# Kernel optimization log

Hardware: AMD Instinct MI355X
Metric: run time of the kernel (lower is better)

Reference implementation:

```python
import jax, jax.numpy as jnp
import numpy as np
from jax import lax

T, D = 8192, 128          # sequence length, feature dim
N_INIT = 100              # burn-in length
RENORM = 0.1
A, B, C = 0.5, 0.9, 0.1   # weighted_dot scaling args: uv = A*gram + B*k_prev + C
EPS = 1e-6                # keep arcsin arg strictly inside (-1, 1)


def kernel_fn(uv, uu, vv):
    # erf-network arcsin kernel
    denom = jnp.sqrt((1.0 + 2.0 * uu) * (1.0 + 2.0 * vv))
    arg = jnp.clip(2.0 * uv / denom, -1.0 + EPS, 1.0 - EPS)
    return (2.0 / jnp.pi) * jnp.arcsin(arg)


def dot_fn(g, k):
    return A * g + B * k + C


def setup_inputs() -> dict:
    key = jax.random.key(0)
    data = jax.random.normal(key, (T, D), dtype=jnp.float32) / np.float32(np.sqrt(D))
    return {"data": data}


def reference(data):
    X = data[:-1]                      # [N, D], N = T - 1
    N = X.shape[0]
    gram = jnp.dot(X, X.T)             # [N, N]
    diag = jnp.diag(gram)              # [N]

    # --- diagonal recursion: scalar carry over time ---
    def diag_step(k_prev, g):
        uv = dot_fn(g, k_prev)
        k = kernel_fn(uv, uv, uv)
        return k, k

    k_diag_final, k_diag = lax.scan(diag_step, jnp.float32(0.0), diag)
    k_diag_shift = jnp.pad(k_diag[:-1], (1, 0))   # shift by one step
    uu = dot_fn(diag, k_diag_shift)               # [N]

    # --- full kernel recursion: carry is a length-N row, shifted each step ---
    def row_step(k_prev, inputs):
        g_row, vv = inputs
        k_prev = jnp.pad(k_prev[:-1], (1, 0))
        uv = dot_fn(g_row, k_prev)
        k = kernel_fn(uv, uu, vv)
        return k, k

    k_final, k_train = lax.scan(row_step, jnp.zeros((N,), jnp.float32), (gram, uu))

    k_train = k_train[N_INIT - 1:, N_INIT - 1:] + RENORM * gram[N_INIT - 1:, N_INIT - 1:]
    return (k_train, uu, k_final, k_diag_final)
```

## Files before the change

kernel.cpp:

```cpp
#include <hip/hip_runtime.h>
#include <hip/hip_fp16.h>

#define N_ROWS 8191
#define NO 8092
#define GSTRIDE 8192
#define SEG 512
#define WARM 96

#define OUT_UU  65480464ul
#define OUT_KF  65488655ul
#define OUT_KDF 65496846ul

#define WS_XB   134217728ul
#define WS_DIAG 136314880ul
#define WS_Q    136347648ul

typedef short bf16x8 __attribute__((ext_vector_type(8)));
typedef float f32x4  __attribute__((ext_vector_type(4)));

__device__ __forceinline__ float asin_core(float a) {
    float ax  = fabsf(a);
    bool  big = ax > 0.5f;
    float z   = big ? 0.5f * (1.0f - ax) : ax * ax;
    float x   = big ? sqrtf(z) : ax;
    float p = fmaf(z, 4.2163199048e-2f, 2.4181311049e-2f);
    p = fmaf(p, z, 4.5470025998e-2f);
    p = fmaf(p, z, 7.4953002686e-2f);
    p = fmaf(p, z, 1.6666752422e-1f);
    p = fmaf(p * z, x, x);
    float r = big ? fmaf(-2.0f, p, 1.57079632679489662f) : p;
    return copysignf(r, a);
}

__device__ __forceinline__ float kstep(float g, float kp, float m) {
    float uv  = fmaf(0.5f, g, fmaf(0.9f, kp, 0.1f));
    float arg = uv * m;
    arg = fminf(fmaxf(arg, -0.999999f), 0.999999f);
    return 0.63661977236758134f * asin_core(arg);
}

__device__ __forceinline__ unsigned short f2bf(float f) {
    unsigned int u = __float_as_uint(f);
    u = (u + 0x7FFFu + ((u >> 16) & 1u)) >> 16;
    return (unsigned short)u;
}

__global__ void k_convert(const float* __restrict__ X, unsigned short* __restrict__ Xb) {
    int idx = blockIdx.x * 256 + threadIdx.x;
    float v = (idx < N_ROWS * 128) ? X[idx] : 0.0f;
    Xb[idx] = f2bf(v);
}

__global__ void k_diag(const float* __restrict__ X, float* __restrict__ diag) {
    int gwave = (blockIdx.x * 256 + threadIdx.x) >> 6;
    int lane  = threadIdx.x & 63;
    if (gwave >= N_ROWS) return;
    const float2* row = (const float2*)(X + (size_t)gwave * 128);
    float2 v = row[lane];
    float s = v.x * v.x + v.y * v.y;
    #pragma unroll
    for (int off = 32; off > 0; off >>= 1) s += __shfl_xor(s, off, 64);
    if (lane == 0) diag[gwave] = s;
}

__global__ void k_scan_diag(const float* __restrict__ diag, float* __restrict__ q,
                            float* __restrict__ d_out) {
    int tid = threadIdx.x;
    int t0  = tid * 32;
    int tw  = max(0, t0 - 32);
    int te  = min(t0 + 32, N_ROWS);
    float kp = 0.0f;
    for (int t = tw; t < te; ++t) {
        float dg = diag[t];
        float uv = fmaf(0.5f, dg, fmaf(0.9f, kp, 0.1f));
        float s  = fabsf(fmaf(2.0f, uv, 1.0f));
        float arg = (uv + uv) / s;
        arg = fminf(fmaxf(arg, -0.999999f), 0.999999f);
        float k = 0.63661977236758134f * asin_core(arg);
        if (t >= t0) {
            d_out[OUT_UU + t] = uv;
            q[t] = 1.0f / sqrtf(s);
            if (t == N_ROWS - 1) d_out[OUT_KDF] = k;
        }
        kp = k;
    }
}

#define GP 136
__global__ __launch_bounds__(256) void k_gemm(const unsigned short* __restrict__ Xb,
                                              __half* __restrict__ gram) {
    int bi = blockIdx.y, bj = blockIdx.x;
    if (bj < bi) return;
    __shared__ short As[128 * GP];
    __shared__ short Bs[128 * GP];
    int tid = threadIdx.x;
    const uint4* ga = (const uint4*)(Xb + (size_t)bi * 128 * 128);
    const uint4* gb = (const uint4*)(Xb + (size_t)bj * 128 * 128);
    #pragma unroll
    for (int p = 0; p < 8; ++p) {
        int chunk = tid + p * 256;
        int row = chunk >> 4, c8 = chunk & 15;
        uint4 va = ga[row * 16 + c8];
        *(uint4*)&As[row * GP + c8 * 8] = va;
        uint4 vb = gb[row * 16 + c8];
        *(uint4*)&Bs[row * GP + c8 * 8] = vb;
    }
    __syncthreads();

    int lane = tid & 63, wave = tid >> 6;
    int wm = wave & 1, wn = wave >> 1;
    int lr = lane & 15, lk = lane >> 4;
    f32x4 acc[4][4];
    #pragma unroll
    for (int mi = 0; mi < 4; ++mi)
        #pragma unroll
        for (int ni = 0; ni < 4; ++ni) acc[mi][ni] = (f32x4){0.f, 0.f, 0.f, 0.f};

    #pragma unroll
    for (int kc = 0; kc < 4; ++kc) {
        bf16x8 a[4], b[4];
        #pragma unroll
        for (int mi = 0; mi < 4; ++mi)
            a[mi] = *(bf16x8*)&As[(wm * 64 + mi * 16 + lr) * GP + kc * 32 + lk * 8];
        #pragma unroll
        for (int ni = 0; ni < 4; ++ni)
            b[ni] = *(bf16x8*)&Bs[(wn * 64 + ni * 16 + lr) * GP + kc * 32 + lk * 8];
        #pragma unroll
        for (int mi = 0; mi < 4; ++mi)
            #pragma unroll
            for (int ni = 0; ni < 4; ++ni)
                acc[mi][ni] = __builtin_amdgcn_mfma_f32_16x16x32_bf16(a[mi], b[ni], acc[mi][ni], 0, 0, 0);
    }

    int row0 = (lane >> 4) * 4, col = lane & 15;
    #pragma unroll
    for (int mi = 0; mi < 4; ++mi) {
        #pragma unroll
        for (int ni = 0; ni < 4; ++ni) {
            size_t gi = (size_t)bi * 128 + wm * 64 + mi * 16 + row0;
            size_t gj = (size_t)bj * 128 + wn * 64 + ni * 16 + col;
            f32x4 v = acc[mi][ni];
            #pragma unroll
            for (int r = 0; r < 4; ++r)
                gram[(gi + r) * GSTRIDE + gj] = __float2half(v[r]);
        }
    }
}

__global__ __launch_bounds__(256) void k_scan_main(const __half* __restrict__ gram,
                                                   const float* __restrict__ q,
                                                   float* __restrict__ d_out) {
    int c = blockIdx.x * 256 + threadIdx.x;
    if (c > NO - 1) return;
    int tlim = N_ROWS - c;
    int t0 = 99 + blockIdx.y * SEG;
    if (t0 >= tlim) return;
    int tend = min(t0 + SEG, tlim);
    int tw = t0 - WARM;

    float kp = 0.0f;
    size_t gidx = (size_t)tw * GSTRIDE + tw + c;
    #pragma unroll 4
    for (int t = tw; t < t0; ++t, gidx += (GSTRIDE + 1)) {
        float g = __half2float(gram[gidx]);
        float m = 2.0f * q[t] * q[t + c];
        kp = kstep(g, kp, m);
    }
    size_t oidx = (size_t)(t0 - 99) * NO + (t0 + c - 99);
    #pragma unroll 4
    for (int t = t0; t < tend; ++t, gidx += (GSTRIDE + 1), oidx += (NO + 1)) {
        float g = __half2float(gram[gidx]);
        float m = 2.0f * q[t] * q[t + c];
        kp = kstep(g, kp, m);
        d_out[oidx] = fmaf(0.1f, g, kp);
    }
    if (tend == tlim) d_out[OUT_KF + (tlim - 1)] = kp;
}

__global__ void k_short_diag(const __half* __restrict__ gram, const float* __restrict__ q,
                             float* __restrict__ d_out) {
    int l = threadIdx.x;
    if (l > 98) return;
    int c = NO + l;
    int tl = N_ROWS - c;
    float kp = 0.0f;
    size_t gidx = (size_t)c;
    for (int t = 0; t < tl; ++t, gidx += (GSTRIDE + 1)) {
        float g = __half2float(gram[gidx]);
        float m = 2.0f * q[t] * q[t + c];
        kp = kstep(g, kp, m);
    }
    d_out[OUT_KF + (tl - 1)] = kp;
}

__global__ __launch_bounds__(256) void k_mirror(float* __restrict__ out) {
    int tc = blockIdx.x, tr = blockIdx.y;
    if (tr < tc) return;
    __shared__ float tile[32][33];
    int tx = threadIdx.x, ty = threadIdx.y;
    int sr0 = tc * 32, sc0 = tr * 32;
    #pragma unroll
    for (int k2 = 0; k2 < 32; k2 += 8) {
        int r = sr0 + ty + k2, cc = sc0 + tx;
        if (r < NO && cc < NO)
            tile[ty + k2][tx] = out[(size_t)r * NO + cc];
    }
    __syncthreads();
    int dr0 = tr * 32, dc0 = tc * 32;
    #pragma unroll
    for (int k2 = 0; k2 < 32; k2 += 8) {
        int r = dr0 + ty + k2, cc = dc0 + tx;
        if (r < NO && cc < NO && r > cc)
            out[(size_t)r * NO + cc] = tile[tx][ty + k2];
    }
}

extern "C" void kernel_launch(void* const* d_in, const int* in_sizes, int n_in,
                              void* d_out, int out_size, void* d_ws, size_t ws_size,
                              hipStream_t stream) {
    const float* X = (const float*)d_in[0];
    float* out = (float*)d_out;
    char* ws = (char*)d_ws;
    __half* gram = (__half*)ws;
    unsigned short* Xb = (unsigned short*)(ws + WS_XB);
    float* diag = (float*)(ws + WS_DIAG);
    float* q = (float*)(ws + WS_Q);

    k_convert<<<dim3(4096), dim3(256), 0, stream>>>(X, Xb);
    k_diag<<<dim3(2048), dim3(256), 0, stream>>>(X, diag);
    k_scan_diag<<<dim3(1), dim3(256), 0, stream>>>(diag, q, out);
    k_gemm<<<dim3(64, 64), dim3(256), 0, stream>>>(Xb, gram);
    k_scan_main<<<dim3(32, 16), dim3(256), 0, stream>>>(gram, q, out);
    k_short_diag<<<dim3(1), dim3(128), 0, stream>>>(gram, q, out);
    k_mirror<<<dim3(253, 253), dim3(32, 8), 0, stream>>>(out);
}
```

Measured before the change: 521.9 us.

## Store gram diagonally skewed, vectorize scan per lane, fuse prep, widen mirror tiles

The GEMM now writes the gram matrix in a skewed layout (row t, offset c = j - i), so the main scan reads contiguous ushort4 vectors per row instead of strided diagonal elements. Each lane now handles four columns, and q values are carried in registers. Segment and warmup lengths shrink to give more parallel blocks. The convert and diag kernels are fused into one, and the mirror transpose uses 64x64 tiles with float4 accesses. Shorter warmup may lose accuracy, and the skewed writes from the GEMM are scattered and less coalesced.

```diff
diff --git a/kernel.cpp b/kernel.cpp
--- a/kernel.cpp
+++ b/kernel.cpp
@@ -4,8 +4,8 @@
 #define N_ROWS 8191
 #define NO 8092
 #define GSTRIDE 8192
-#define SEG 512
-#define WARM 96
+#define SEG 128
+#define WARM 24
 
 #define OUT_UU  65480464ul
 #define OUT_KF  65488655ul
@@ -17,12 +17,16 @@
 
 typedef short bf16x8 __attribute__((ext_vector_type(8)));
 typedef float f32x4  __attribute__((ext_vector_type(4)));
+
+__device__ __forceinline__ float h2f(unsigned short u) {
+    __half_raw r; r.x = u; return __half2float(__half(r));
+}
 
 __device__ __forceinline__ float asin_core(float a) {
     float ax  = fabsf(a);
     bool  big = ax > 0.5f;
     float z   = big ? 0.5f * (1.0f - ax) : ax * ax;
-    float x   = big ? sqrtf(z) : ax;
+    float x   = big ? __builtin_amdgcn_sqrtf(z) : ax;
     float p = fmaf(z, 4.2163199048e-2f, 2.4181311049e-2f);
     p = fmaf(p, z, 4.5470025998e-2f);
     p = fmaf(p, z, 7.4953002686e-2f);
@@ -45,22 +49,20 @@
     return (unsigned short)u;
 }
 
-__global__ void k_convert(const float* __restrict__ X, unsigned short* __restrict__ Xb) {
-    int idx = blockIdx.x * 256 + threadIdx.x;
-    float v = (idx < N_ROWS * 128) ? X[idx] : 0.0f;
-    Xb[idx] = f2bf(v);
-}
-
-__global__ void k_diag(const float* __restrict__ X, float* __restrict__ diag) {
-    int gwave = (blockIdx.x * 256 + threadIdx.x) >> 6;
-    int lane  = threadIdx.x & 63;
-    if (gwave >= N_ROWS) return;
-    const float2* row = (const float2*)(X + (size_t)gwave * 128);
-    float2 v = row[lane];
-    float s = v.x * v.x + v.y * v.y;
-    #pragma unroll
-    for (int off = 32; off > 0; off >>= 1) s += __shfl_xor(s, off, 64);
-    if (lane == 0) diag[gwave] = s;
+__global__ void k_prep(const float* __restrict__ X, unsigned short* __restrict__ Xb,
+                       float* __restrict__ diag) {
+    int gw = (blockIdx.x * 256 + threadIdx.x) >> 6;
+    int lane = threadIdx.x & 63;
+    float2 v = make_float2(0.0f, 0.0f);
+    if (gw < N_ROWS) v = ((const float2*)(X + (size_t)gw * 128))[lane];
+    ushort2 b; b.x = f2bf(v.x); b.y = f2bf(v.y);
+    ((ushort2*)(Xb + (size_t)gw * 128))[lane] = b;
+    if (gw < N_ROWS) {
+        float s = v.x * v.x + v.y * v.y;
+        #pragma unroll
+        for (int off = 32; off > 0; off >>= 1) s += __shfl_xor(s, off, 64);
+        if (lane == 0) diag[gw] = s;
+    }
 }
 
 __global__ void k_scan_diag(const float* __restrict__ diag, float* __restrict__ q,
@@ -84,6 +86,7 @@
         }
         kp = k;
     }
+    for (int j = tid; j < 1024; j += 256) q[N_ROWS + j] = 1.0f;
 }
 
 #define GP 136
@@ -137,81 +140,147 @@
     for (int mi = 0; mi < 4; ++mi) {
         #pragma unroll
         for (int ni = 0; ni < 4; ++ni) {
-            size_t gi = (size_t)bi * 128 + wm * 64 + mi * 16 + row0;
-            size_t gj = (size_t)bj * 128 + wn * 64 + ni * 16 + col;
+            int gi0 = bi * 128 + wm * 64 + mi * 16 + row0;
+            int gj  = bj * 128 + wn * 64 + ni * 16 + col;
             f32x4 v = acc[mi][ni];
             #pragma unroll
-            for (int r = 0; r < 4; ++r)
-                gram[(gi + r) * GSTRIDE + gj] = __float2half(v[r]);
-        }
-    }
-}
-
-__global__ __launch_bounds__(256) void k_scan_main(const __half* __restrict__ gram,
-                                                   const float* __restrict__ q,
-                                                   float* __restrict__ d_out) {
-    int c = blockIdx.x * 256 + threadIdx.x;
-    if (c > NO - 1) return;
-    int tlim = N_ROWS - c;
+            for (int r = 0; r < 4; ++r) {
+                int gi = gi0 + r, c = gj - gi;
+                if (c >= 0)
+                    gram[(size_t)gi * GSTRIDE + c] = __float2half(v[r]);
+            }
+        }
+    }
+}
+
+__global__ __launch_bounds__(64) void k_scan_main(const unsigned short* __restrict__ gram,
+                                                  const float* __restrict__ q,
+                                                  float* __restrict__ d_out) {
+    int lane = threadIdx.x;
+    int cbase = blockIdx.x * 256;
+    int cl = cbase + lane * 4;
+    int tlimw = N_ROWS - cbase;
     int t0 = 99 + blockIdx.y * SEG;
-    if (t0 >= tlim) return;
-    int tend = min(t0 + SEG, tlim);
+    if (t0 >= tlimw) return;
+    int tend = min(t0 + SEG, tlimw);
     int tw = t0 - WARM;
-
-    float kp = 0.0f;
-    size_t gidx = (size_t)tw * GSTRIDE + tw + c;
-    #pragma unroll 4
-    for (int t = tw; t < t0; ++t, gidx += (GSTRIDE + 1)) {
-        float g = __half2float(gram[gidx]);
-        float m = 2.0f * q[t] * q[t + c];
-        kp = kstep(g, kp, m);
-    }
-    size_t oidx = (size_t)(t0 - 99) * NO + (t0 + c - 99);
-    #pragma unroll 4
-    for (int t = t0; t < tend; ++t, gidx += (GSTRIDE + 1), oidx += (NO + 1)) {
-        float g = __half2float(gram[gidx]);
-        float m = 2.0f * q[t] * q[t + c];
-        kp = kstep(g, kp, m);
-        d_out[oidx] = fmaf(0.1f, g, kp);
-    }
-    if (tend == tlim) d_out[OUT_KF + (tlim - 1)] = kp;
-}
-
-__global__ void k_short_diag(const __half* __restrict__ gram, const float* __restrict__ q,
-                             float* __restrict__ d_out) {
+    int tl0 = N_ROWS - cl;
+
+    float k0 = 0.f, k1 = 0.f, k2 = 0.f, k3 = 0.f;
+    float q0 = q[tw + cl], q1 = q[tw + cl + 1], q2 = q[tw + cl + 2], q3 = q[tw + cl + 3];
+    const ushort4* gp = (const ushort4*)(gram + (size_t)tw * GSTRIDE + cl);
+
+    for (int t = tw; t < t0; ++t) {
+        ushort4 gv = *gp;
+        float qt2 = q[t] * 2.0f;
+        k0 = kstep(h2f(gv.x), k0, qt2 * q0);
+        k1 = kstep(h2f(gv.y), k1, qt2 * q1);
+        k2 = kstep(h2f(gv.z), k2, qt2 * q2);
+        k3 = kstep(h2f(gv.w), k3, qt2 * q3);
+        q0 = q1; q1 = q2; q2 = q3; q3 = q[t + cl + 4];
+        gp += GSTRIDE / 4;
+    }
+    float* orow = d_out + (size_t)(t0 - 99) * NO + (t0 + cl - 99);
+    if (tend + 256 <= tlimw) {
+        for (int t = t0; t < tend; ++t) {
+            ushort4 gv = *gp;
+            float qt2 = q[t] * 2.0f;
+            float g0 = h2f(gv.x), g1 = h2f(gv.y), g2 = h2f(gv.z), g3 = h2f(gv.w);
+            k0 = kstep(g0, k0, qt2 * q0);
+            k1 = kstep(g1, k1, qt2 * q1);
+            k2 = kstep(g2, k2, qt2 * q2);
+            k3 = kstep(g3, k3, qt2 * q3);
+            orow[0] = fmaf(0.1f, g0, k0);
+            orow[1] = fmaf(0.1f, g1, k1);
+            orow[2] = fmaf(0.1f, g2, k2);
+            orow[3] = fmaf(0.1f, g3, k3);
+            q0 = q1; q1 = q2; q2 = q3; q3 = q[t + cl + 4];
+            gp += GSTRIDE / 4; orow += NO + 1;
+        }
+    } else {
+        for (int t = t0; t < tend; ++t) {
+            ushort4 gv = *gp;
+            float qt2 = q[t] * 2.0f;
+            float g0 = h2f(gv.x), g1 = h2f(gv.y), g2 = h2f(gv.z), g3 = h2f(gv.w);
+            k0 = kstep(g0, k0, qt2 * q0);
+            k1 = kstep(g1, k1, qt2 * q1);
+            k2 = kstep(g2, k2, qt2 * q2);
+            k3 = kstep(g3, k3, qt2 * q3);
+            if (t < tl0    ) orow[0] = fmaf(0.1f, g0, k0);
+            if (t < tl0 - 1) orow[1] = fmaf(0.1f, g1, k1);
+            if (t < tl0 - 2) orow[2] = fmaf(0.1f, g2, k2);
+            if (t < tl0 - 3) orow[3] = fmaf(0.1f, g3, k3);
+            if (t == tl0 - 1) d_out[OUT_KF + t] = k0;
+            if (t == tl0 - 2) d_out[OUT_KF + t] = k1;
+            if (t == tl0 - 3) d_out[OUT_KF + t] = k2;
+            if (t == tl0 - 4) d_out[OUT_KF + t] = k3;
+            q0 = q1; q1 = q2; q2 = q3; q3 = q[t + cl + 4];
+            gp += GSTRIDE / 4; orow += NO + 1;
+        }
+    }
+}
+
+__global__ void k_short_diag(const unsigned short* __restrict__ gram,
+                             const float* __restrict__ q, float* __restrict__ d_out) {
     int l = threadIdx.x;
     if (l > 98) return;
     int c = NO + l;
     int tl = N_ROWS - c;
     float kp = 0.0f;
-    size_t gidx = (size_t)c;
-    for (int t = 0; t < tl; ++t, gidx += (GSTRIDE + 1)) {
-        float g = __half2float(gram[gidx]);
+    for (int t = 0; t < tl; ++t) {
+        float g = h2f(gram[(size_t)t * GSTRIDE + c]);
         float m = 2.0f * q[t] * q[t + c];
         kp = kstep(g, kp, m);
     }
     d_out[OUT_KF + (tl - 1)] = kp;
 }
 
+#define MT 64
 __global__ __launch_bounds__(256) void k_mirror(float* __restrict__ out) {
     int tc = blockIdx.x, tr = blockIdx.y;
     if (tr < tc) return;
-    __shared__ float tile[32][33];
-    int tx = threadIdx.x, ty = threadIdx.y;
-    int sr0 = tc * 32, sc0 = tr * 32;
-    #pragma unroll
-    for (int k2 = 0; k2 < 32; k2 += 8) {
-        int r = sr0 + ty + k2, cc = sc0 + tx;
-        if (r < NO && cc < NO)
-            tile[ty + k2][tx] = out[(size_t)r * NO + cc];
+    __shared__ float tile[MT][MT + 1];
+    int tid = threadIdx.x;
+    int x4 = (tid & 15) * 4, yy = tid >> 4;
+    int sr = tc * MT, scol = tr * MT;
+    bool interior = (scol + MT <= NO);
+    if (interior) {
+        #pragma unroll
+        for (int k = 0; k < 4; ++k) {
+            int r = yy + 16 * k;
+            float4 v = *(const float4*)&out[(size_t)(sr + r) * NO + scol + x4];
+            tile[x4 + 0][r] = v.x; tile[x4 + 1][r] = v.y;
+            tile[x4 + 2][r] = v.z; tile[x4 + 3][r] = v.w;
+        }
+    } else {
+        for (int k = 0; k < 4; ++k) {
+            int r = yy + 16 * k;
+            for (int j = 0; j < 4; ++j) {
+                int rr = sr + r, cc = scol + x4 + j;
+                tile[x4 + j][r] = (rr < NO && cc < NO) ? out[(size_t)rr * NO + cc] : 0.0f;
+            }
+        }
     }
     __syncthreads();
-    int dr0 = tr * 32, dc0 = tc * 32;
-    #pragma unroll
-    for (int k2 = 0; k2 < 32; k2 += 8) {
-        int r = dr0 + ty + k2, cc = dc0 + tx;
-        if (r < NO && cc < NO && r > cc)
-            out[(size_t)r * NO + cc] = tile[tx][ty + k2];
+    int dr = tr * MT, dcol = tc * MT;
+    if (interior && tr != tc) {
+        #pragma unroll
+        for (int k = 0; k < 4; ++k) {
+            int r = yy + 16 * k;
+            float4 v;
+            v.x = tile[r][x4 + 0]; v.y = tile[r][x4 + 1];
+            v.z = tile[r][x4 + 2]; v.w = tile[r][x4 + 3];
+            *(float4*)&out[(size_t)(dr + r) * NO + dcol + x4] = v;
+        }
+    } else {
+        for (int k = 0; k < 4; ++k) {
+            int r = yy + 16 * k;
+            for (int j = 0; j < 4; ++j) {
+                int rr = dr + r, cc = dcol + x4 + j;
+                if (rr < NO && cc < NO && rr > cc)
+                    out[(size_t)rr * NO + cc] = tile[r][x4 + j];
+            }
+        }
     }
 }
 
@@ -226,11 +295,10 @@
     float* diag = (float*)(ws + WS_DIAG);
     float* q = (float*)(ws + WS_Q);
 
-    k_convert<<<dim3(4096), dim3(256), 0, stream>>>(X, Xb);
-    k_diag<<<dim3(2048), dim3(256), 0, stream>>>(X, diag);
+    k_prep<<<dim3(2048), dim3(256), 0, stream>>>(X, Xb, diag);
     k_scan_diag<<<dim3(1), dim3(256), 0, stream>>>(diag, q, out);
     k_gemm<<<dim3(64, 64), dim3(256), 0, stream>>>(Xb, gram);
-    k_scan_main<<<dim3(32, 16), dim3(256), 0, stream>>>(gram, q, out);
-    k_short_diag<<<dim3(1), dim3(128), 0, stream>>>(gram, q, out);
-    k_mirror<<<dim3(253, 253), dim3(32, 8), 0, stream>>>(out);
-}
+    k_scan_main<<<dim3(32, 64), dim3(64), 0, stream>>>((const unsigned short*)gram, q, out);
+    k_short_diag<<<dim3(1), dim3(128), 0, stream>>>((const unsigned short*)gram, q, out);
+    k_mirror<<<dim3(127, 127), dim3(256), 0, stream>>>(out);
+}
```

After: 551.8 us. 5.7% more time.
